# Performance work log

Hardware: AMD Instinct MI355X
Metric: run time of the kernel (lower is better)

The kernel has to match this reference:

```python
import jax, jax.numpy as jnp
import numpy as np

TOP_K = 6  # num_experts_per_tok


def _glu_mlp(x, wg, wu, wd):
    # DeepSeek MLP: down( silu(gate(x)) * up(x) )
    return (jax.nn.silu(x @ wg) * (x @ wu)) @ wd


def setup_inputs() -> dict:
    key = jax.random.key(0)
    ks = jax.random.split(key, 8)
    B, S, D, E, F, FS = 2, 2048, 1024, 8, 512, 1024
    sc = 0.02
    return {
        "hidden_states": jax.random.normal(ks[0], (B, S, D), jnp.float32),
        "router_w": jax.random.normal(ks[1], (D, E), jnp.float32) * sc,
        "w_gate": jax.random.normal(ks[2], (E, D, F), jnp.float32) * sc,
        "w_up": jax.random.normal(ks[3], (E, D, F), jnp.float32) * sc,
        "w_down": jax.random.normal(ks[4], (E, F, D), jnp.float32) * sc,
        "ws_gate": jax.random.normal(ks[5], (D, FS), jnp.float32) * sc,
        "ws_up": jax.random.normal(ks[6], (D, FS), jnp.float32) * sc,
        "ws_down": jax.random.normal(ks[7], (FS, D), jnp.float32) * sc,
    }


def reference(hidden_states, router_w, w_gate, w_up, w_down, ws_gate, ws_up, ws_down):
    B, S, D = hidden_states.shape
    x = hidden_states.reshape(-1, D)                       # [T, D] tokens
    # Gate: softmax router + top-k (DeepSeek gate, no renorm)
    scores = jax.nn.softmax(x @ router_w, axis=-1)         # [T, E]
    topk_w, topk_idx = jax.lax.top_k(scores, TOP_K)        # [T, K]
    # Expert SiLU-GLU MLPs evaluated for all experts (math-identical to the
    # argsort dispatch -> grouped GEMM -> scatter combine in moe_infer)
    g = jnp.einsum('td,edf->etf', x, w_gate)               # [E, T, F]
    u = jnp.einsum('td,edf->etf', x, w_up)                 # [E, T, F]
    f_all = jnp.einsum('etf,efd->ted', jax.nn.silu(g) * u, w_down)  # [T, E, D]
    # Combine: final[t] = sum_k topk_w[t,k] * expert_{topk_idx[t,k]}(x[t])
    picked = jnp.take_along_axis(f_all, topk_idx[:, :, None], axis=1)  # [T, K, D]
    y = jnp.sum(picked * topk_w[:, :, None], axis=1).reshape(B, S, D)
    # shared experts branch
    y = y + _glu_mlp(hidden_states, ws_gate, ws_up, ws_down)
    return y
```

## Files before the change

### kernel.cpp

```cpp
#include <hip/hip_runtime.h>

typedef __attribute__((ext_vector_type(8))) short bf16x8;
typedef __attribute__((ext_vector_type(4))) float floatx4;

static __device__ __forceinline__ float b2f(unsigned short u) {
  union { unsigned int i; float f; } v; v.i = ((unsigned int)u) << 16; return v.f;
}
static __device__ __forceinline__ unsigned short f2b(float f) {
  union { float f; unsigned int i; } v; v.f = f;
  unsigned int x = v.i;
  return (unsigned short)((x + 0x7fffu + ((x >> 16) & 1u)) >> 16);
}

#define GLDS(gp, lp) \
  __builtin_amdgcn_global_load_lds( \
      (const __attribute__((address_space(1))) unsigned int*)(gp), \
      (__attribute__((address_space(3))) unsigned int*)(lp), 16, 0, 0)

static __device__ __forceinline__ void swizzle_mn(int lin, int Mb, int Nb,
                                                  int& m_idx, int& n_idx) {
  if ((Mb & 7) == 0) {
    int xcd = lin & 7;
    int idx = lin >> 3;
    int nstrips = Mb >> 3;
    m_idx = (idx % nstrips) * 8 + xcd;
    n_idx = idx / nstrips;
  } else {
    m_idx = lin % Mb;
    n_idx = lin / Mb;
  }
}

__global__ void cvt_f32_bf16(const float* __restrict__ src,
                             unsigned short* __restrict__ dst) {
  int i = (blockIdx.x * 256 + threadIdx.x) * 4;
  float4 v = *(const float4*)(src + i);
  ushort4 o;
  o.x = f2b(v.x); o.y = f2b(v.y); o.z = f2b(v.z); o.w = f2b(v.w);
  *(ushort4*)(dst + i) = o;
}

__global__ void transpose_f32_bf16_2(const float* __restrict__ sA,
                                     unsigned short* __restrict__ dA, int nzA,
                                     const float* __restrict__ sB,
                                     unsigned short* __restrict__ dB,
                                     int K, int N) {
  __shared__ unsigned short tile[32][33];
  int z = blockIdx.z;
  const float* src;
  unsigned short* dst;
  if (z < nzA) { src = sA + (size_t)z * K * N; dst = dA + (size_t)z * K * N; }
  else { src = sB + (size_t)(z - nzA) * K * N; dst = dB + (size_t)(z - nzA) * K * N; }
  const int bx = blockIdx.x * 32;
  const int by = blockIdx.y * 32;
  const int tx = threadIdx.x, ty = threadIdx.y;
#pragma unroll
  for (int i = 0; i < 4; i++)
    tile[ty + i * 8][tx] = f2b(src[(size_t)(by + ty + i * 8) * N + bx + tx]);
  __syncthreads();
#pragma unroll
  for (int i = 0; i < 4; i++)
    dst[(size_t)(bx + ty + i * 8) * K + by + tx] = tile[tx][ty + i * 8];
}

__global__ void transpose3_1024(const float* __restrict__ s0,
                                const float* __restrict__ s1,
                                const float* __restrict__ s2,
                                unsigned short* __restrict__ d0,
                                unsigned short* __restrict__ d1,
                                unsigned short* __restrict__ d2) {
  __shared__ unsigned short tile[32][33];
  const float* src = (blockIdx.z == 0) ? s0 : (blockIdx.z == 1) ? s1 : s2;
  unsigned short* dst = (blockIdx.z == 0) ? d0 : (blockIdx.z == 1) ? d1 : d2;
  const int bx = blockIdx.x * 32;
  const int by = blockIdx.y * 32;
  const int tx = threadIdx.x, ty = threadIdx.y;
#pragma unroll
  for (int i = 0; i < 4; i++)
    tile[ty + i * 8][tx] = f2b(src[(size_t)(by + ty + i * 8) * 1024 + bx + tx]);
  __syncthreads();
#pragma unroll
  for (int i = 0; i < 4; i++)
    dst[(size_t)(bx + ty + i * 8) * 1024 + by + tx] = tile[tx][ty + i * 8];
}

__global__ void router_topk(const float* __restrict__ X,
                            const float* __restrict__ RW,
                            float* __restrict__ cw) {
  const int t = blockIdx.x;
  const int lane = threadIdx.x;
  float acc[8];
#pragma unroll
  for (int e = 0; e < 8; e++) acc[e] = 0.f;
  for (int d = lane; d < 1024; d += 64) {
    float xv = X[(size_t)t * 1024 + d];
    const float* r = RW + d * 8;
    float4 r0 = *(const float4*)r;
    float4 r1 = *(const float4*)(r + 4);
    acc[0] += xv * r0.x; acc[1] += xv * r0.y;
    acc[2] += xv * r0.z; acc[3] += xv * r0.w;
    acc[4] += xv * r1.x; acc[5] += xv * r1.y;
    acc[6] += xv * r1.z; acc[7] += xv * r1.w;
  }
#pragma unroll
  for (int m = 1; m < 64; m <<= 1) {
#pragma unroll
    for (int e = 0; e < 8; e++) acc[e] += __shfl_xor(acc[e], m);
  }
  if (lane == 0) {
    float mx = acc[0];
#pragma unroll
    for (int e = 1; e < 8; e++) mx = fmaxf(mx, acc[e]);
    float prob[8], s = 0.f;
#pragma unroll
    for (int e = 0; e < 8; e++) { prob[e] = expf(acc[e] - mx); s += prob[e]; }
    float inv = 1.f / s;
#pragma unroll
    for (int e = 0; e < 8; e++) prob[e] *= inv;
    int m1 = 0;
#pragma unroll
    for (int e = 1; e < 8; e++) if (prob[e] < prob[m1]) m1 = e;
    int m2 = -1;
#pragma unroll
    for (int e = 0; e < 8; e++)
      if (e != m1 && (m2 < 0 || prob[e] < prob[m2])) m2 = e;
#pragma unroll
    for (int e = 0; e < 8; e++)
      cw[(size_t)t * 8 + e] = (e == m1 || e == m2) ? 0.f : prob[e];
  }
}

#define VMCNT(N) asm volatile("s_waitcnt vmcnt(" #N ")" ::: "memory")
#define BARS() do { __builtin_amdgcn_s_barrier(); \
                    __builtin_amdgcn_sched_barrier(0); } while (0)

#define STG_I0(K, BS) do { \
  GLDS(a0 + (K),          sm + (BS) + wid * 512); \
  GLDS(a0 + (K) + 131072, sm + (BS) + 8192 + wid * 512); } while (0)
#define STG_I1(K, BS) do { \
  GLDS(bg0 + (K),        sm + (BS) + 16384 + wid * 1024); \
  GLDS(bg0 + (K) + 8192, sm + (BS) + 16384 + wid * 1024 + 512); } while (0)
#define STG_I2(K, BS) do { \
  GLDS(bu0 + (K),        sm + (BS) + 24576 + wid * 1024); \
  GLDS(bu0 + (K) + 8192, sm + (BS) + 24576 + wid * 1024 + 512); } while (0)
#define STG_I3(K, BS) do { \
  GLDS(a0 + (K) + 65536,  sm + (BS) + 4096 + wid * 512); \
  GLDS(a0 + (K) + 196608, sm + (BS) + 12288 + wid * 512); } while (0)

#define READ_A(DST, DB, H) do { _Pragma("unroll") \
  for (int mf = 0; mf < 4; ++mf) { \
    const int row_ = wm * 128 + (H) * 64 + mf * 16 + lr; \
    const int rb_ = (DB) + row_ * 64; const int rx_ = row_ & 7; \
    DST[mf][0] = *(const bf16x8*)(sm + rb_ + ((quad ^ rx_) << 3)); \
    DST[mf][1] = *(const bf16x8*)(sm + rb_ + (((4 + quad) ^ rx_) << 3)); \
  } } while (0)

#define READ_B(DST, DB, RG) do { _Pragma("unroll") \
  for (int nf = 0; nf < 2; ++nf) { \
    const int row_ = wn * 32 + nf * 16 + lr; \
    const int rb_ = (DB) + (RG) + row_ * 64; const int rx_ = row_ & 7; \
    DST[nf][0] = *(const bf16x8*)(sm + rb_ + ((quad ^ rx_) << 3)); \
    DST[nf][1] = *(const bf16x8*)(sm + rb_ + (((4 + quad) ^ rx_) << 3)); \
  } } while (0)

#define MM(ACC, AF, BF) do { \
  __builtin_amdgcn_s_setprio(1); \
  _Pragma("unroll") \
  for (int mf = 0; mf < 4; ++mf) { _Pragma("unroll") \
    for (int nf = 0; nf < 2; ++nf) { \
      ACC[mf][nf] = __builtin_amdgcn_mfma_f32_16x16x32_bf16( \
          AF[mf][0], BF[nf][0], ACC[mf][nf], 0, 0, 0); \
      ACC[mf][nf] = __builtin_amdgcn_mfma_f32_16x16x32_bf16( \
          AF[mf][1], BF[nf][1], ACC[mf][nf], 0, 0, 0); \
    } } \
  __builtin_amdgcn_s_setprio(0); } while (0)

__global__ __launch_bounds__(512, 2) void gemm_gu_fused(
    const unsigned short* __restrict__ X,
    const unsigned short* __restrict__ WgTe,
    const unsigned short* __restrict__ WgTs,
    const unsigned short* __restrict__ WuTe,
    const unsigned short* __restrict__ WuTs,
    unsigned short* __restrict__ H,
    const float* __restrict__ cw, int Mb) {
  __shared__ __align__(16) unsigned short sm[65536];
  const int tid = threadIdx.x;
  const int wid = tid >> 6, lane = tid & 63;
  const int lr = lane & 15, quad = lane >> 4;
  const int wm = wid >> 2, wn = wid & 3;

  int m_idx, n_idx;
  {
    int lin = blockIdx.x;
    if ((Mb & 7) == 0) {
      int xcd = lin & 7, idx = lin >> 3;
      n_idx = idx % 40;
      m_idx = (idx / 40) * 8 + xcd;
    } else {
      m_idx = lin % Mb;
      n_idx = lin / Mb;
    }
  }
  const int m0 = m_idx * 256;
  const int n0 = n_idx * 128;

  const unsigned short *Bg, *Bu;
  int eidx = -1;
  if (n0 < 4096) {
    eidx = n0 >> 9;
    size_t off = ((size_t)eidx * 512 + (n0 & 511)) * 1024;
    Bg = WgTe + off; Bu = WuTe + off;
  } else {
    size_t off = (size_t)(n0 - 4096) * 1024;
    Bg = WgTs + off; Bu = WuTs + off;
  }

  const int grow8 = lane >> 3;
  const int gcol = ((lane & 7) ^ grow8) << 3;
  const unsigned short* a0 =
      X + (size_t)(m0 + wid * 8 + grow8) * 1024 + gcol;
  const unsigned short* bg0 =
      Bg + (size_t)(wid * 16 + grow8) * 1024 + gcol;
  const unsigned short* bu0 =
      Bu + (size_t)(wid * 16 + grow8) * 1024 + gcol;

  floatx4 gg[2][4][2], uu[2][4][2];
#pragma unroll
  for (int h = 0; h < 2; h++)
#pragma unroll
    for (int mf = 0; mf < 4; mf++)
#pragma unroll
      for (int nf = 0; nf < 2; nf++) {
        gg[h][mf][nf] = (floatx4)0.f;
        uu[h][mf][nf] = (floatx4)0.f;
      }

  bf16x8 fA0[4][2], fA1[4][2], fBg[2][2], fBu[2][2];

  STG_I0(0, 0); STG_I1(0, 0); STG_I2(0, 0); STG_I3(0, 0);

  for (int t = 0; t < 15; ++t) {
    const int db = (t & 1) << 15;
    const int nb = 32768 - db;
    const int kn = (t + 1) * 64;
    STG_I0(kn, nb);
    VMCNT(6); BARS();
    READ_A(fA0, db, 0);
    READ_B(fBg, db, 16384);
    MM(gg[0], fA0, fBg);
    STG_I1(kn, nb);
    VMCNT(6); BARS();
    READ_B(fBu, db, 24576);
    MM(uu[0], fA0, fBu);
    STG_I2(kn, nb);
    VMCNT(6); BARS();
    READ_A(fA1, db, 1);
    MM(gg[1], fA1, fBg);
    STG_I3(kn, nb);
    BARS();
    MM(uu[1], fA1, fBu);
  }
  {
    const int db = 32768;
    VMCNT(4); BARS();
    READ_A(fA0, db, 0);
    READ_B(fBg, db, 16384);
    MM(gg[0], fA0, fBg);
    VMCNT(2); BARS();
    READ_B(fBu, db, 24576);
    MM(uu[0], fA0, fBu);
    VMCNT(0); BARS();
    READ_A(fA1, db, 1);
    MM(gg[1], fA1, fBg);
    MM(uu[1], fA1, fBu);
  }

#pragma unroll
  for (int h = 0; h < 2; h++) {
#pragma unroll
    for (int mf = 0; mf < 4; mf++) {
#pragma unroll
      for (int nf = 0; nf < 2; nf++) {
#pragma unroll
        for (int r = 0; r < 4; r++) {
          int row = m0 + wm * 128 + h * 64 + mf * 16 + quad * 4 + r;
          int col = n0 + wn * 32 + nf * 16 + lr;
          float g = gg[h][mf][nf][r];
          float u = uu[h][mf][nf][r];
          float s = (eidx >= 0) ? cw[(size_t)row * 8 + eidx] : 1.0f;
          float silu = g / (1.0f + __expf(-g));
          H[(size_t)row * 5120 + col] = f2b(s * silu * u);
        }
      }
    }
  }
}

__global__ __launch_bounds__(256) void gemm_down(
    const unsigned short* __restrict__ H,
    const unsigned short* __restrict__ WdTe,
    const unsigned short* __restrict__ WdTs,
    float* __restrict__ Y, int Mb) {
  __shared__ __align__(16) unsigned short lA[128 * 64];
  __shared__ __align__(16) unsigned short lB[64 * 64];
  const int tid = threadIdx.x;
  const int wid = tid >> 6, lane = tid & 63;
  const int lr = lane & 15, quad = lane >> 4;
  const int wm = wid >> 1, wn = wid & 1;
  int m_idx, n_idx;
  swizzle_mn(blockIdx.x, Mb, 16, m_idx, n_idx);
  const int m0 = m_idx * 128;
  const int n0 = n_idx * 64;

  floatx4 acc[4][2];
#pragma unroll
  for (int i = 0; i < 4; i++)
#pragma unroll
    for (int j = 0; j < 2; j++) acc[i][j] = (floatx4)0.f;

  for (int k0 = 0; k0 < 5120; k0 += 64) {
    __syncthreads();
#pragma unroll
    for (int i = 0; i < 4; i++) {
      int c = i * 256 + tid;
      int row = c >> 3;
      int g = ((c & 7) ^ (row & 7)) << 3;
      GLDS(H + (size_t)(m0 + row) * 5120 + k0 + g,
           lA + (size_t)(i * 256 + wid * 64) * 8);
    }
#pragma unroll
    for (int i = 0; i < 2; i++) {
      int c = i * 256 + tid;
      int row = c >> 3;
      int g = ((c & 7) ^ (row & 7)) << 3;
      const unsigned short* gpb;
      if (k0 < 4096) {
        gpb = WdTe + (size_t)(k0 >> 9) * (1024 * 512) +
              (size_t)(n0 + row) * 512 + (k0 & 511) + g;
      } else {
        gpb = WdTs + (size_t)(n0 + row) * 1024 + (k0 - 4096) + g;
      }
      GLDS(gpb, lB + (size_t)(i * 256 + wid * 64) * 8);
    }
    __syncthreads();
    bf16x8 af[4][2], bfr[2][2];
#pragma unroll
    for (int mt = 0; mt < 4; mt++) {
      int row = wm * 64 + mt * 16 + lr;
#pragma unroll
      for (int kt = 0; kt < 2; kt++)
        af[mt][kt] = *(const bf16x8*)(lA + row * 64 +
                                      ((((kt << 2) + quad) ^ (row & 7)) << 3));
    }
#pragma unroll
    for (int nt = 0; nt < 2; nt++) {
      int row = wn * 32 + nt * 16 + lr;
#pragma unroll
      for (int kt = 0; kt < 2; kt++)
        bfr[nt][kt] = *(const bf16x8*)(lB + row * 64 +
                                       ((((kt << 2) + quad) ^ (row & 7)) << 3));
    }
#pragma unroll
    for (int kt = 0; kt < 2; kt++)
#pragma unroll
      for (int mt = 0; mt < 4; mt++)
#pragma unroll
        for (int nt = 0; nt < 2; nt++)
          acc[mt][nt] = __builtin_amdgcn_mfma_f32_16x16x32_bf16(
              af[mt][kt], bfr[nt][kt], acc[mt][nt], 0, 0, 0);
  }

#pragma unroll
  for (int mt = 0; mt < 4; mt++)
#pragma unroll
    for (int nt = 0; nt < 2; nt++)
#pragma unroll
      for (int r = 0; r < 4; r++) {
        int row = m0 + wm * 64 + mt * 16 + quad * 4 + r;
        int col = n0 + wn * 32 + nt * 16 + lr;
        Y[(size_t)row * 1024 + col] = acc[mt][nt][r];
      }
}

extern "C" void kernel_launch(void* const* d_in, const int* in_sizes, int n_in,
                              void* d_out, int out_size, void* d_ws, size_t ws_size,
                              hipStream_t stream) {
  const float* hs  = (const float*)d_in[0];
  const float* rw  = (const float*)d_in[1];
  const float* wg  = (const float*)d_in[2];
  const float* wu  = (const float*)d_in[3];
  const float* wd  = (const float*)d_in[4];
  const float* wsg = (const float*)d_in[5];
  const float* wsu = (const float*)d_in[6];
  const float* wsd = (const float*)d_in[7];
  float* out = (float*)d_out;

  char* p = (char*)d_ws;
  float* cw = (float*)p;                    p += (size_t)4096 * 8 * 4;
  unsigned short* Xb   = (unsigned short*)p; p += (size_t)4096 * 1024 * 2;
  unsigned short* wgT  = (unsigned short*)p; p += (size_t)8 * 512 * 1024 * 2;
  unsigned short* wuT  = (unsigned short*)p; p += (size_t)8 * 512 * 1024 * 2;
  unsigned short* wsgT = (unsigned short*)p; p += (size_t)1024 * 1024 * 2;
  unsigned short* wsuT = (unsigned short*)p; p += (size_t)1024 * 1024 * 2;
  unsigned short* wdT  = (unsigned short*)p; p += (size_t)8 * 1024 * 512 * 2;
  unsigned short* wsdT = (unsigned short*)p; p += (size_t)1024 * 1024 * 2;
  unsigned short* GH   = (unsigned short*)p;
  const size_t base_bytes = (size_t)(p - (char*)d_ws);

  int chunks = 8;
  for (int c = 1; c <= 8; c *= 2) {
    size_t gh_bytes = ((size_t)4096 / c) * 5120 * 2;
    if (base_bytes + gh_bytes <= ws_size) { chunks = c; break; }
  }
  const int rows = 4096 / chunks;
  const int Mb = rows / 128;
  const int MbG = rows / 256;

  dim3 tb(32, 8);
  cvt_f32_bf16<<<4096, 256, 0, stream>>>(hs, Xb);
  router_topk<<<4096, 64, 0, stream>>>(hs, rw, cw);
  transpose_f32_bf16_2<<<dim3(16, 32, 16), tb, 0, stream>>>(
      wg, wgT, 8, wu, wuT, 1024, 512);
  transpose_f32_bf16_2<<<dim3(32, 16, 8), tb, 0, stream>>>(
      wd, wdT, 8, wd, wdT, 512, 1024);
  transpose3_1024<<<dim3(32, 32, 3), tb, 0, stream>>>(
      wsg, wsu, wsd, wsgT, wsuT, wsdT);

  for (int c = 0; c < chunks; c++) {
    const unsigned short* Xc = Xb + (size_t)c * rows * 1024;
    const float* cwc = cw + (size_t)c * rows * 8;
    float* outc = out + (size_t)c * rows * 1024;
    gemm_gu_fused<<<MbG * 40, 512, 0, stream>>>(
        Xc, wgT, wsgT, wuT, wsuT, GH, cwc, MbG);
    gemm_down<<<Mb * 16, 256, 0, stream>>>(GH, wdT, wsdT, outc, Mb);
  }
}
```

Measured before the change: 309.9 us.

## Pipeline down-projection GEMM with triple-buffered LDS and larger 128x128 tiles

Rewrites the down-projection GEMM so each block computes a 128x128 output tile with 8 waves instead of 128x64 with 4, halving the number of blocks and the re-reads of H. The K loop becomes a triple-buffered global-to-LDS pipeline that prefetches two tiles ahead, with vmcnt waits and barriers instead of two full syncs per step. MFMA sections run at raised wave priority. It uses 96KB of LDS per block, which limits occupancy, and relies on VMCNT/BARS macros assumed to exist elsewhere in the file.

New measurement: 292.8 us. -5.5%, faster.

```diff
diff --git a/kernel.cpp b/kernel.cpp
--- a/kernel.cpp
+++ b/kernel.cpp
@@ -296,21 +296,69 @@
   }
 }
 
-__global__ __launch_bounds__(256) void gemm_down(
+#define DN_STG(KN, SBUF) do { \
+  GLDS(Ha + (size_t)(KN),          smD + (SBUF) + wid * 512); \
+  GLDS(Ha + (size_t)(KN) + 327680, smD + (SBUF) + 4096 + wid * 512); \
+  const unsigned short *b0p_, *b1p_; \
+  if ((KN) < 4096) { \
+    const unsigned short* be_ = WdTe + ((size_t)((KN) >> 9)) * (1024 * 512) + ((KN) & 511); \
+    b0p_ = be_ + (size_t)bn0 * 512 + gcol; \
+    b1p_ = be_ + (size_t)(bn0 + 64) * 512 + gcol; \
+  } else { \
+    b0p_ = WdTs + (size_t)bn0 * 1024 + ((KN) - 4096) + gcol; \
+    b1p_ = WdTs + (size_t)(bn0 + 64) * 1024 + ((KN) - 4096) + gcol; \
+  } \
+  GLDS(b0p_, smD + (SBUF) + 8192 + wid * 512); \
+  GLDS(b1p_, smD + (SBUF) + 12288 + wid * 512); } while (0)
+
+#define DN_TILE(T, BUF, SBUF, DOSTG, VM) do { \
+  VMCNT(VM); BARS(); \
+  if (DOSTG) { DN_STG(((T) + 2) * 64, SBUF); } \
+  bf16x8 af_[4][2], bf_[2][2]; \
+  _Pragma("unroll") \
+  for (int mt = 0; mt < 4; ++mt) { \
+    const int row_ = wm * 64 + mt * 16 + lr; \
+    const int rb_ = (BUF) + row_ * 64; const int rx_ = row_ & 7; \
+    af_[mt][0] = *(const bf16x8*)(smD + rb_ + ((quad ^ rx_) << 3)); \
+    af_[mt][1] = *(const bf16x8*)(smD + rb_ + (((4 + quad) ^ rx_) << 3)); \
+  } \
+  _Pragma("unroll") \
+  for (int nt = 0; nt < 2; ++nt) { \
+    const int row_ = wn * 32 + nt * 16 + lr; \
+    const int rb_ = (BUF) + 8192 + row_ * 64; const int rx_ = row_ & 7; \
+    bf_[nt][0] = *(const bf16x8*)(smD + rb_ + ((quad ^ rx_) << 3)); \
+    bf_[nt][1] = *(const bf16x8*)(smD + rb_ + (((4 + quad) ^ rx_) << 3)); \
+  } \
+  __builtin_amdgcn_s_setprio(1); \
+  _Pragma("unroll") \
+  for (int kt = 0; kt < 2; ++kt) \
+    _Pragma("unroll") \
+    for (int mt = 0; mt < 4; ++mt) \
+      _Pragma("unroll") \
+      for (int nt = 0; nt < 2; ++nt) \
+        acc[mt][nt] = __builtin_amdgcn_mfma_f32_16x16x32_bf16( \
+            af_[mt][kt], bf_[nt][kt], acc[mt][nt], 0, 0, 0); \
+  __builtin_amdgcn_s_setprio(0); } while (0)
+
+__global__ __launch_bounds__(512, 2) void gemm_down(
     const unsigned short* __restrict__ H,
     const unsigned short* __restrict__ WdTe,
     const unsigned short* __restrict__ WdTs,
     float* __restrict__ Y, int Mb) {
-  __shared__ __align__(16) unsigned short lA[128 * 64];
-  __shared__ __align__(16) unsigned short lB[64 * 64];
+  __shared__ __align__(16) unsigned short smD[49152];
   const int tid = threadIdx.x;
   const int wid = tid >> 6, lane = tid & 63;
   const int lr = lane & 15, quad = lane >> 4;
-  const int wm = wid >> 1, wn = wid & 1;
+  const int wm = wid >> 2, wn = wid & 3;
   int m_idx, n_idx;
-  swizzle_mn(blockIdx.x, Mb, 16, m_idx, n_idx);
+  swizzle_mn(blockIdx.x, Mb, 8, m_idx, n_idx);
   const int m0 = m_idx * 128;
-  const int n0 = n_idx * 64;
+  const int n0 = n_idx * 128;
+
+  const int grow8 = lane >> 3;
+  const int gcol = ((lane & 7) ^ grow8) << 3;
+  const unsigned short* Ha = H + (size_t)(m0 + wid * 8 + grow8) * 5120 + gcol;
+  const int bn0 = n0 + wid * 8 + grow8;
 
   floatx4 acc[4][2];
 #pragma unroll
@@ -318,57 +366,16 @@
 #pragma unroll
     for (int j = 0; j < 2; j++) acc[i][j] = (floatx4)0.f;
 
-  for (int k0 = 0; k0 < 5120; k0 += 64) {
-    __syncthreads();
-#pragma unroll
-    for (int i = 0; i < 4; i++) {
-      int c = i * 256 + tid;
-      int row = c >> 3;
-      int g = ((c & 7) ^ (row & 7)) << 3;
-      GLDS(H + (size_t)(m0 + row) * 5120 + k0 + g,
-           lA + (size_t)(i * 256 + wid * 64) * 8);
-    }
-#pragma unroll
-    for (int i = 0; i < 2; i++) {
-      int c = i * 256 + tid;
-      int row = c >> 3;
-      int g = ((c & 7) ^ (row & 7)) << 3;
-      const unsigned short* gpb;
-      if (k0 < 4096) {
-        gpb = WdTe + (size_t)(k0 >> 9) * (1024 * 512) +
-              (size_t)(n0 + row) * 512 + (k0 & 511) + g;
-      } else {
-        gpb = WdTs + (size_t)(n0 + row) * 1024 + (k0 - 4096) + g;
-      }
-      GLDS(gpb, lB + (size_t)(i * 256 + wid * 64) * 8);
-    }
-    __syncthreads();
-    bf16x8 af[4][2], bfr[2][2];
-#pragma unroll
-    for (int mt = 0; mt < 4; mt++) {
-      int row = wm * 64 + mt * 16 + lr;
-#pragma unroll
-      for (int kt = 0; kt < 2; kt++)
-        af[mt][kt] = *(const bf16x8*)(lA + row * 64 +
-                                      ((((kt << 2) + quad) ^ (row & 7)) << 3));
-    }
-#pragma unroll
-    for (int nt = 0; nt < 2; nt++) {
-      int row = wn * 32 + nt * 16 + lr;
-#pragma unroll
-      for (int kt = 0; kt < 2; kt++)
-        bfr[nt][kt] = *(const bf16x8*)(lB + row * 64 +
-                                       ((((kt << 2) + quad) ^ (row & 7)) << 3));
-    }
-#pragma unroll
-    for (int kt = 0; kt < 2; kt++)
-#pragma unroll
-      for (int mt = 0; mt < 4; mt++)
-#pragma unroll
-        for (int nt = 0; nt < 2; nt++)
-          acc[mt][nt] = __builtin_amdgcn_mfma_f32_16x16x32_bf16(
-              af[mt][kt], bfr[nt][kt], acc[mt][nt], 0, 0, 0);
-  }
+  DN_STG(0, 0);
+  DN_STG(64, 16384);
+
+  for (int t = 0; t < 78; t += 3) {
+    DN_TILE(t,     0,     32768, true, 4);
+    DN_TILE(t + 1, 16384, 0,     true, 4);
+    DN_TILE(t + 2, 32768, 16384, true, 4);
+  }
+  DN_TILE(78, 0,     0, false, 4);
+  DN_TILE(79, 16384, 0, false, 0);
 
 #pragma unroll
   for (int mt = 0; mt < 4; mt++)
@@ -432,6 +439,6 @@
     float* outc = out + (size_t)c * rows * 1024;
     gemm_gu_fused<<<MbG * 40, 512, 0, stream>>>(
         Xc, wgT, wsgT, wuT, wsuT, GH, cwc, MbG);
-    gemm_down<<<Mb * 16, 256, 0, stream>>>(GH, wdT, wsdT, outc, Mb);
-  }
-}
+    gemm_down<<<Mb * 8, 512, 0, stream>>>(GH, wdT, wsdT, outc, Mb);
+  }
+}
```
